# Kernel tuning notes

Hardware: AMD Instinct MI355X
Metric: run time of the kernel (lower is better)

Reference implementation:

```python
import jax, jax.numpy as jnp
import numpy as np

N, B, DIN = 128, 2, 128
D, DFF, NHEAD, NLAYERS = 256, 1024, 8, 2
BLOCK = 32
LENGTH = 160


def setup_inputs() -> dict:
    key = jax.random.key(0)
    ks = jax.random.split(key, 10)
    r = lambda k, sh: jax.random.normal(k, sh, jnp.float32) * 0.05
    return {
        "inputs": jax.random.normal(ks[0], (N, B, DIN), jnp.float32),
        "in_W1": r(ks[1], (DIN, DFF)), "in_b1": jnp.zeros((DFF,), jnp.float32),
        "in_W2": r(ks[2], (DFF, D)), "in_b2": jnp.zeros((D,), jnp.float32),
        "k_W1": r(ks[3], (DIN, DFF)), "k_b1": jnp.zeros((DFF,), jnp.float32),
        "k_W2": r(ks[4], (DFF, 2)), "k_b2": jnp.zeros((2,), jnp.float32),
        "Wqkv": r(ks[5], (NLAYERS, D, 3 * D)), "bqkv": jnp.zeros((NLAYERS, 3 * D), jnp.float32),
        "Wo": r(ks[6], (NLAYERS, D, D)), "bo": jnp.zeros((NLAYERS, D), jnp.float32),
        "ln1_g": jnp.ones((NLAYERS, D), jnp.float32), "ln1_b": jnp.zeros((NLAYERS, D), jnp.float32),
        "W1": r(ks[7], (NLAYERS, D, DFF)), "b1": jnp.zeros((NLAYERS, DFF), jnp.float32),
        "W2": r(ks[8], (NLAYERS, DFF, D)), "b2": jnp.zeros((NLAYERS, D), jnp.float32),
        "ln2_g": jnp.ones((NLAYERS, D), jnp.float32), "ln2_b": jnp.zeros((NLAYERS, D), jnp.float32),
        "length": LENGTH,
    }


def _ln(x, g, b):
    m = jnp.mean(x, axis=-1, keepdims=True)
    v = jnp.mean(jnp.square(x - m), axis=-1, keepdims=True)
    return (x - m) * jax.lax.rsqrt(v + 1e-5) * g + b


def _forward(inputs, in_W1, in_b1, in_W2, in_b2, k_W1, k_b1, k_W2, k_b2,
             Wqkv, bqkv, Wo, bo, ln1_g, ln1_b, W1, b1, W2, b2, ln2_g, ln2_b, length):
    n, b, din = inputs.shape
    d = in_W2.shape[1]
    H, dh = NHEAD, in_W2.shape[1] // NHEAD
    Wmax = 2 * BLOCK + 1
    L = length
    idx = jnp.arange(n)
    starts = jnp.maximum(0, idx - BLOCK)                 # [N]
    ends = jnp.minimum(L, idx + BLOCK + 1)               # [N]
    cols = starts[:, None] + jnp.arange(Wmax)[None, :]   # [N,Wmax] absolute column per window slot
    valid = cols < ends[:, None]                          # [N,Wmax] ragged-window mask

    # sinusoidal PE at absolute column positions (start_idx = max(0, i-block))
    pos = cols.astype(jnp.float32)
    div = jnp.exp(jnp.arange(0, din, 2, dtype=jnp.float32) * (-np.log(10000.0) / din))
    ang = pos[..., None] * div                            # [N,Wmax,din/2]
    pe = jnp.stack([jnp.sin(ang), jnp.cos(ang)], axis=-1).reshape(n, Wmax, din)

    # row token repeated across its window + PE, then input_ff
    x = inputs[:, None, :, :] + pe[:, :, None, :]         # [N,Wmax,B,din]
    h = jnp.maximum(x @ in_W1 + in_b1, 0.0) @ in_W2 + in_b2  # [N,Wmax,B,D]

    # TransformerEncoder (post-norm, relu, eval mode) over the window axis, padded slots masked as keys
    kmask = valid[:, None, None, None, :]                 # [N,1,1,1,Wmax]
    scale = 1.0 / np.sqrt(dh)
    for l in range(Wqkv.shape[0]):
        qkv = h @ Wqkv[l] + bqkv[l]
        q, k, v = [t.reshape(n, Wmax, b, H, dh) for t in jnp.split(qkv, 3, axis=-1)]
        s = jnp.einsum('nqbhe,nkbhe->nbhqk', q, k) * scale
        s = jnp.where(kmask, s, -jnp.inf)
        a = jax.nn.softmax(s, axis=-1)
        o = jnp.einsum('nbhqk,nkbhe->nqbhe', a, v).reshape(n, Wmax, b, d)
        h = _ln(h + o @ Wo[l] + bo[l], ln1_g[l], ln1_b[l])
        f = jnp.maximum(h @ W1[l] + b1[l], 0.0) @ W2[l] + b2[l]
        h = _ln(h + f, ln2_g[l], ln2_b[l])

    # hierarchy kernel scores (Gaussian band kernel with learned (mu, logsig) per row/batch)
    kp = jnp.maximum(inputs @ k_W1 + k_b1, 0.0) @ k_W2 + k_b2   # [N,B,2]
    hscale = L / n
    diff = cols.astype(jnp.float32) - idx[:, None].astype(jnp.float32) * hscale  # [N,Wmax]
    hier = -jnp.square(diff[:, :, None] - kp[:, None, :, 0]) * jnp.exp(kp[:, None, :, 1])  # [N,Wmax,B]

    # scatter banded values/scores into dense [N,L,...] then row-softmax and weighted combine
    n_idx = jnp.broadcast_to(idx[:, None], (n, Wmax))
    scat = jnp.where(valid, cols, L)                      # out-of-bounds -> dropped
    v_mat = jnp.zeros((n, L, b, d), jnp.float32).at[n_idx, scat].set(h, mode='drop')
    h_mat = jnp.full((n, L, b), -jnp.inf, jnp.float32).at[n_idx, scat].set(hier, mode='drop')
    w = jax.nn.softmax(h_mat, axis=0)[..., None]          # softmax over rows per column
    return jnp.sum(v_mat * w, axis=0)                     # [L,B,D]


def reference(inputs, in_W1, in_b1, in_W2, in_b2, k_W1, k_b1, k_W2, k_b2,
              Wqkv, bqkv, Wo, bo, ln1_g, ln1_b, W1, b1, W2, b2, ln2_g, ln2_b, length):
    return _forward(inputs, in_W1, in_b1, in_W2, in_b2, k_W1, k_b1, k_W2, k_b2,
                    Wqkv, bqkv, Wo, bo, ln1_g, ln1_b, W1, b1, W2, b2, ln2_g, ln2_b, length)
```

## Files before the change

### kernel.cpp

```cpp
#include <hip/hip_runtime.h>

constexpr int NN    = 128;
constexpr int BB    = 2;
constexpr int DIN   = 128;
constexpr int DD    = 256;
constexpr int DFF   = 1024;
constexpr int NH    = 8;
constexpr int DH    = 32;
constexpr int NL    = 2;
constexpr int BLK   = 32;
constexpr int WMAX  = 2 * BLK + 1;
constexpr int RROWS = NN * WMAX * BB;

typedef __attribute__((ext_vector_type(8))) short s16x8;
typedef __attribute__((ext_vector_type(4))) float f32x4;

__device__ __forceinline__ ushort f2bf(float f) {
  unsigned u = __float_as_uint(f);
  unsigned r = (u + 0x7fffu + ((u >> 16) & 1u)) >> 16;
  return (ushort)r;
}
__device__ __forceinline__ float bf2f(ushort h) {
  return __uint_as_float(((unsigned)h) << 16);
}
__device__ __forceinline__ float bfl(unsigned u) { return __uint_as_float(u << 16); }
__device__ __forceinline__ float bfh(unsigned u) { return __uint_as_float(u & 0xffff0000u); }

struct TD { const float* in; ushort* out; int K; int N; };
struct TPack { TD d[10]; };

__global__ __launch_bounds__(256) void k_wconv(TPack p) {
  TD t = p.d[blockIdx.y];
  int total = t.K * t.N;
  for (int i = blockIdx.x * 256 + threadIdx.x; i < total; i += gridDim.x * 256) {
    int n = i / t.K, k = i - n * t.K;
    t.out[i] = f2bf(t.in[(size_t)k * t.N + n]);
  }
}

__global__ __launch_bounds__(256) void k_buildx(const float* __restrict__ inp,
                                                ushort* __restrict__ x) {
  int e = blockIdx.x * 256 + threadIdx.x;
  int i = e & 127, r = e >> 7;
  int n = r / (WMAX * BB);
  int rem = r - n * (WMAX * BB);
  int w = rem >> 1, b = rem & 1;
  int st = n - BLK; if (st < 0) st = 0;
  float pos = (float)(st + w);
  float div = __expf(-0.0719557841f * (float)(i & 126));
  float ang = pos * div;
  float pe = (i & 1) ? __cosf(ang) : __sinf(ang);
  x[e] = f2bf(inp[(n * BB + b) * DIN + i] + pe);
}

__global__ __launch_bounds__(256) void k_kp(
    const float* __restrict__ inp, const float* __restrict__ kW1,
    const float* __restrict__ kb1, const float* __restrict__ kW2,
    const float* __restrict__ kb2, float* __restrict__ kp) {
  __shared__ float xs[DIN];
  __shared__ float red[8];
  int row = blockIdx.x;
  int tid = threadIdx.x;
  if (tid < DIN) xs[tid] = inp[row * DIN + tid];
  __syncthreads();
  float a0 = 0.f, a1 = 0.f;
  for (int j = tid; j < DFF; j += 256) {
    float acc = kb1[j];
    for (int k = 0; k < DIN; ++k) acc += xs[k] * kW1[k * DFF + j];
    acc = fmaxf(acc, 0.f);
    a0 += acc * kW2[2 * j];
    a1 += acc * kW2[2 * j + 1];
  }
#pragma unroll
  for (int m = 32; m > 0; m >>= 1) {
    a0 += __shfl_xor(a0, m, 64);
    a1 += __shfl_xor(a1, m, 64);
  }
  if ((tid & 63) == 0) { red[(tid >> 6) * 2] = a0; red[(tid >> 6) * 2 + 1] = a1; }
  __syncthreads();
  if (tid == 0) {
    kp[row * 2 + 0] = red[0] + red[2] + red[4] + red[6] + kb2[0];
    kp[row * 2 + 1] = red[1] + red[3] + red[5] + red[7] + kb2[1];
  }
}

constexpr int BM = 128, BN = 64, BK = 64;

template<int RELU, int HAS_RES>
__global__ __launch_bounds__(256) void k_gemm(
    const ushort* __restrict__ A, const ushort* __restrict__ Bt,
    const float* __restrict__ bias, const ushort* __restrict__ resid,
    ushort* __restrict__ out, int N, int K) {
  __shared__ __align__(16) char As[BM * BK * 2];
  __shared__ __align__(16) char Bs[BN * BK * 2];
  int tid = threadIdx.x;
  int m0 = blockIdx.x * BM, n0 = blockIdx.y * BN;
  int lane = tid & 63, w = tid >> 6;
  int wr = w >> 1, wc = w & 1;
  int fr = lane & 15, g = lane >> 4;
  f32x4 acc[4][2] = {};

  for (int kb = 0; kb < K; kb += BK) {
    __syncthreads();
#pragma unroll
    for (int it = 0; it < 4; ++it) {
      int e = tid + it * 256;
      int row = e >> 3, c = e & 7;
      uint4 v = *(const uint4*)(A + (size_t)(m0 + row) * K + kb + c * 8);
      int boff = (row * 128 + c * 16) ^ ((row & 7) << 4);
      *(uint4*)(As + boff) = v;
    }
#pragma unroll
    for (int it = 0; it < 2; ++it) {
      int e = tid + it * 256;
      int row = e >> 3, c = e & 7;
      uint4 v = *(const uint4*)(Bt + (size_t)(n0 + row) * K + kb + c * 8);
      int boff = (row * 128 + c * 16) ^ ((row & 7) << 4);
      *(uint4*)(Bs + boff) = v;
    }
    __syncthreads();
#pragma unroll
    for (int ks = 0; ks < 2; ++ks) {
      int kByte = ks * 64 + g * 16;
      s16x8 a[4], b[2];
#pragma unroll
      for (int m = 0; m < 4; ++m) {
        int row = wr * 64 + m * 16 + fr;
        a[m] = *(const s16x8*)(As + ((row * 128 + kByte) ^ ((row & 7) << 4)));
      }
#pragma unroll
      for (int n = 0; n < 2; ++n) {
        int row = wc * 32 + n * 16 + fr;
        b[n] = *(const s16x8*)(Bs + ((row * 128 + kByte) ^ ((row & 7) << 4)));
      }
#pragma unroll
      for (int m = 0; m < 4; ++m)
#pragma unroll
        for (int n = 0; n < 2; ++n)
          acc[m][n] = __builtin_amdgcn_mfma_f32_16x16x32_bf16(a[m], b[n], acc[m][n], 0, 0, 0);
    }
  }
#pragma unroll
  for (int m = 0; m < 4; ++m) {
    int row = m0 + wr * 64 + m * 16 + g * 4;
#pragma unroll
    for (int n = 0; n < 2; ++n) {
      int col = n0 + wc * 32 + n * 16 + fr;
      float bv = bias[col];
#pragma unroll
      for (int j = 0; j < 4; ++j) {
        float v = acc[m][n][j] + bv;
        if (HAS_RES) v += bf2f(resid[(size_t)(row + j) * N + col]);
        if (RELU) v = fmaxf(v, 0.f);
        out[(size_t)(row + j) * N + col] = f2bf(v);
      }
    }
  }
}

constexpr int QKS = 40;
constexpr int VTS = 104;
constexpr int PS  = 104;

__global__ __launch_bounds__(320) void k_attn(
    const ushort* __restrict__ qkv, ushort* __restrict__ o,
    const int* __restrict__ lenp) {
  __shared__ __align__(16) ushort Qs[80 * QKS];
  __shared__ __align__(16) ushort Ks[80 * QKS];
  __shared__ __align__(16) ushort Vt[32 * VTS];
  __shared__ __align__(16) ushort Pb[5 * 16 * PS];
  int L = lenp[0];
  int blk = blockIdx.x;
  int hh = blk & 7;
  int nb = blk >> 3;
  int b = nb & 1;
  int n = nb >> 1;
  int s0 = n - BLK; if (s0 < 0) s0 = 0;
  int e0 = n + BLK + 1; if (e0 > L) e0 = L;
  int vn = e0 - s0;
  int tid = threadIdx.x;

  for (int i = tid; i < 32 * VTS / 2; i += 320) ((uint*)Vt)[i] = 0;
  for (int i = tid; i < 15 * QKS / 2; i += 320) {
    ((uint*)(Qs + 65 * QKS))[i] = 0;
    ((uint*)(Ks + 65 * QKS))[i] = 0;
  }
  for (int e = tid; e < 65 * 4; e += 320) {
    int r = e >> 2, c = e & 3;
    const ushort* base = qkv + ((size_t)(n * WMAX + r) * BB + b) * (3 * DD) + hh * DH;
    *(uint4*)(Qs + r * QKS + c * 8) = *(const uint4*)(base + c * 8);
    *(uint4*)(Ks + r * QKS + c * 8) = *(const uint4*)(base + DD + c * 8);
    uint4 vv = *(const uint4*)(base + 2 * DD + c * 8);
    const ushort* vp = (const ushort*)&vv;
#pragma unroll
    for (int u = 0; u < 8; ++u) Vt[(c * 8 + u) * VTS + r] = vp[u];
  }
  __syncthreads();

  int w = tid >> 6, lane = tid & 63;
  int fr = lane & 15, g = lane >> 4;
  int q0 = w * 16;
  ushort* Pw = Pb + w * 16 * PS;

  s16x8 aq = *(const s16x8*)(Qs + (q0 + fr) * QKS + g * 8);
  f32x4 sacc[5];
#pragma unroll
  for (int t = 0; t < 5; ++t) {
    s16x8 bk = *(const s16x8*)(Ks + (t * 16 + fr) * QKS + g * 8);
    f32x4 z = {0.f, 0.f, 0.f, 0.f};
    sacc[t] = __builtin_amdgcn_mfma_f32_16x16x32_bf16(aq, bk, z, 0, 0, 0);
  }
  const float scl = 0.17677669529663687f;
#pragma unroll
  for (int j = 0; j < 4; ++j) {
    float pv[5];
    float mx = -3e38f;
#pragma unroll
    for (int t = 0; t < 5; ++t) {
      bool ok = (t * 16 + fr) < vn;
      pv[t] = ok ? sacc[t][j] * scl : -3e38f;
      mx = fmaxf(mx, pv[t]);
    }
#pragma unroll
    for (int d = 1; d < 16; d <<= 1) mx = fmaxf(mx, __shfl_xor(mx, d, 64));
    float sum = 0.f;
#pragma unroll
    for (int t = 0; t < 5; ++t) {
      float e = ((t * 16 + fr) < vn) ? __expf(pv[t] - mx) : 0.f;
      pv[t] = e;
      sum += e;
    }
#pragma unroll
    for (int d = 1; d < 16; d <<= 1) sum += __shfl_xor(sum, d, 64);
    float inv = 1.f / sum;
#pragma unroll
    for (int t = 0; t < 5; ++t)
      Pw[(g * 4 + j) * PS + t * 16 + fr] = f2bf(pv[t] * inv);
  }
  {
    int zr = lane >> 2, zc = 80 + (lane & 3) * 4;
    *(uint2*)(Pw + zr * PS + zc) = make_uint2(0u, 0u);
  }
  __syncthreads();

  f32x4 oacc[2] = {};
#pragma unroll
  for (int k0 = 0; k0 < 3; ++k0) {
    s16x8 ap = *(const s16x8*)(Pw + fr * PS + k0 * 32 + g * 8);
#pragma unroll
    for (int nt = 0; nt < 2; ++nt) {
      s16x8 bv = *(const s16x8*)(Vt + (nt * 16 + fr) * VTS + k0 * 32 + g * 8);
      oacc[nt] = __builtin_amdgcn_mfma_f32_16x16x32_bf16(ap, bv, oacc[nt], 0, 0, 0);
    }
  }
#pragma unroll
  for (int nt = 0; nt < 2; ++nt) {
#pragma unroll
    for (int j = 0; j < 4; ++j) {
      int qr = q0 + g * 4 + j;
      if (qr < WMAX)
        o[((size_t)(n * WMAX + qr) * BB + b) * DD + hh * DH + nt * 16 + fr] =
            f2bf(oacc[nt][j]);
    }
  }
}

__global__ __launch_bounds__(256) void k_ln(
    const ushort* __restrict__ z, const float* __restrict__ g,
    const float* __restrict__ be, ushort* __restrict__ h) {
  int row = blockIdx.x * 4 + (threadIdx.x >> 6);
  int lane = threadIdx.x & 63;
  const ushort* zr = z + (size_t)row * DD + lane * 4;
  uint2 pk = *(const uint2*)zr;
  float v0 = bfl(pk.x), v1 = bfh(pk.x), v2 = bfl(pk.y), v3 = bfh(pk.y);
  float sm = v0 + v1 + v2 + v3;
  float sq = v0 * v0 + v1 * v1 + v2 * v2 + v3 * v3;
#pragma unroll
  for (int m = 32; m > 0; m >>= 1) {
    sm += __shfl_xor(sm, m, 64);
    sq += __shfl_xor(sq, m, 64);
  }
  float mean = sm * (1.f / DD);
  float var = sq * (1.f / DD) - mean * mean;
  float rs = rsqrtf(var + 1e-5f);
  int c = lane * 4;
  float o0 = (v0 - mean) * rs * g[c] + be[c];
  float o1 = (v1 - mean) * rs * g[c + 1] + be[c + 1];
  float o2 = (v2 - mean) * rs * g[c + 2] + be[c + 2];
  float o3 = (v3 - mean) * rs * g[c + 3] + be[c + 3];
  uint2 outp;
  outp.x = (unsigned)f2bf(o0) | ((unsigned)f2bf(o1) << 16);
  outp.y = (unsigned)f2bf(o2) | ((unsigned)f2bf(o3) << 16);
  *(uint2*)(h + (size_t)row * DD + c) = outp;
}

__global__ __launch_bounds__(256) void k_final(
    const ushort* __restrict__ h, const float* __restrict__ kp,
    float* __restrict__ out, const int* __restrict__ lenp) {
  int L = lenp[0];
  int t = blockIdx.x >> 1, b = blockIdx.x & 1;
  float hsc = (float)L / (float)NN;
  int nlo = t - BLK; if (nlo < 0) nlo = 0;
  int nhi = t + BLK; if (nhi > NN - 1) nhi = NN - 1;
  float mx = -3e38f;
  for (int n = nlo; n <= nhi; ++n) {
    float kp0 = kp[(n * BB + b) * 2 + 0];
    float kp1 = kp[(n * BB + b) * 2 + 1];
    float dif = (float)t - (float)n * hsc - kp0;
    float lg = -dif * dif * __expf(kp1);
    mx = fmaxf(mx, lg);
  }
  float sum = 0.f, acc = 0.f;
  int c = threadIdx.x;
  for (int n = nlo; n <= nhi; ++n) {
    float kp0 = kp[(n * BB + b) * 2 + 0];
    float kp1 = kp[(n * BB + b) * 2 + 1];
    float dif = (float)t - (float)n * hsc - kp0;
    float lg = -dif * dif * __expf(kp1);
    float p = __expf(lg - mx);
    sum += p;
    int st = n - BLK; if (st < 0) st = 0;
    int w = t - st;
    acc += p * bf2f(h[(size_t)((n * WMAX + w) * BB + b) * DD + c]);
  }
  out[(size_t)(t * BB + b) * DD + c] = acc / sum;
}

extern "C" void kernel_launch(void* const* d_in, const int* in_sizes, int n_in,
                              void* d_out, int out_size, void* d_ws, size_t ws_size,
                              hipStream_t stream) {
  const float* inputs = (const float*)d_in[0];
  const float* in_W1  = (const float*)d_in[1];
  const float* in_b1  = (const float*)d_in[2];
  const float* in_W2  = (const float*)d_in[3];
  const float* in_b2  = (const float*)d_in[4];
  const float* k_W1   = (const float*)d_in[5];
  const float* k_b1   = (const float*)d_in[6];
  const float* k_W2   = (const float*)d_in[7];
  const float* k_b2   = (const float*)d_in[8];
  const float* Wqkv   = (const float*)d_in[9];
  const float* bqkv   = (const float*)d_in[10];
  const float* Wo     = (const float*)d_in[11];
  const float* bo     = (const float*)d_in[12];
  const float* ln1_g  = (const float*)d_in[13];
  const float* ln1_b  = (const float*)d_in[14];
  const float* W1     = (const float*)d_in[15];
  const float* b1     = (const float*)d_in[16];
  const float* W2     = (const float*)d_in[17];
  const float* b2     = (const float*)d_in[18];
  const float* ln2_g  = (const float*)d_in[19];
  const float* ln2_b  = (const float*)d_in[20];
  const int*   lenp   = (const int*)d_in[21];
  float* out = (float*)d_out;
  (void)in_sizes; (void)n_in; (void)ws_size;

  ushort* wsu = (ushort*)d_ws;
  size_t off = 0;
  auto alloc = [&](size_t nelem) { ushort* p = wsu + off; off += (nelem + 7) & ~7ull; return p; };
  ushort* inW1t = alloc((size_t)DFF * DIN);
  ushort* inW2t = alloc((size_t)DD * DFF);
  ushort* Wqkvt = alloc((size_t)NL * 3 * DD * DD);
  ushort* Wot   = alloc((size_t)NL * DD * DD);
  ushort* W1t   = alloc((size_t)NL * DFF * DD);
  ushort* W2t   = alloc((size_t)NL * DD * DFF);
  ushort* xz    = alloc((size_t)RROWS * DD);
  ushort* tq    = alloc((size_t)RROWS * DFF);
  ushort* hb    = alloc((size_t)RROWS * DD);
  ushort* ob    = alloc((size_t)RROWS * DD);
  float*  kp    = (float*)(wsu + off);

  int L = out_size / (BB * DD);

  TPack tp;
  tp.d[0] = {in_W1, inW1t, DIN, DFF};
  tp.d[1] = {in_W2, inW2t, DFF, DD};
  tp.d[2] = {Wqkv,                       Wqkvt,                     DD, 3 * DD};
  tp.d[3] = {Wqkv + (size_t)DD * 3 * DD, Wqkvt + (size_t)3 * DD * DD, DD, 3 * DD};
  tp.d[4] = {Wo,                    Wot,                  DD, DD};
  tp.d[5] = {Wo + (size_t)DD * DD,  Wot + (size_t)DD * DD, DD, DD};
  tp.d[6] = {W1,                     W1t,                   DD, DFF};
  tp.d[7] = {W1 + (size_t)DD * DFF,  W1t + (size_t)DFF * DD, DD, DFF};
  tp.d[8] = {W2,                     W2t,                   DFF, DD};
  tp.d[9] = {W2 + (size_t)DFF * DD,  W2t + (size_t)DD * DFF, DFF, DD};
  k_wconv<<<dim3(1024, 10), 256, 0, stream>>>(tp);

  k_buildx<<<RROWS * DIN / 256, 256, 0, stream>>>(inputs, xz);
  k_kp<<<NN * BB, 256, 0, stream>>>(inputs, k_W1, k_b1, k_W2, k_b2, kp);

  k_gemm<1, 0><<<dim3(RROWS / BM, DFF / BN), 256, 0, stream>>>(
      xz, inW1t, in_b1, nullptr, tq, DFF, DIN);
  k_gemm<0, 0><<<dim3(RROWS / BM, DD / BN), 256, 0, stream>>>(
      tq, inW2t, in_b2, nullptr, hb, DD, DFF);

  for (int l = 0; l < NL; ++l) {
    k_gemm<0, 0><<<dim3(RROWS / BM, 3 * DD / BN), 256, 0, stream>>>(
        hb, Wqkvt + (size_t)l * 3 * DD * DD, bqkv + (size_t)l * 3 * DD,
        nullptr, tq, 3 * DD, DD);
    k_attn<<<NN * BB * NH, 320, 0, stream>>>(tq, ob, lenp);
    k_gemm<0, 1><<<dim3(RROWS / BM, DD / BN), 256, 0, stream>>>(
        ob, Wot + (size_t)l * DD * DD, bo + (size_t)l * DD, hb, xz, DD, DD);
    k_ln<<<RROWS / 4, 256, 0, stream>>>(xz, ln1_g + (size_t)l * DD,
                                        ln1_b + (size_t)l * DD, hb);
    k_gemm<1, 0><<<dim3(RROWS / BM, DFF / BN), 256, 0, stream>>>(
        hb, W1t + (size_t)l * DFF * DD, b1 + (size_t)l * DFF, nullptr, tq, DFF, DD);
    k_gemm<0, 1><<<dim3(RROWS / BM, DD / BN), 256, 0, stream>>>(
        tq, W2t + (size_t)l * DD * DFF, b2 + (size_t)l * DD, hb, xz, DD, DFF);
    k_ln<<<RROWS / 4, 256, 0, stream>>>(xz, ln2_g + (size_t)l * DD,
                                        ln2_b + (size_t)l * DD, hb);
  }
  k_final<<<L * BB, 256, 0, stream>>>(hb, kp, out, lenp);
}
```

Baseline: 323.7 us.

## Fuse LayerNorm into full-width GEMM epilogue and retile GEMMs to 512 threads

Replaces the 256-thread 128x64 GEMM with a 512-thread kernel whose tiles span 256 output columns. For the output-projection and FFN-down GEMMs, each block then covers a whole 256-wide row, so the bias, residual add and LayerNorm run in the epilogue. This removes the separate k_ln launches and the intermediate xz round trip to global memory. The weight-conversion kernel also becomes a shared-memory tiled transpose for coalesced reads and writes. The cost is fewer blocks for the N=256 GEMMs, plus an in-place residual/output on hb that relies on each block reading its residual before the barrier and writing after it.

```diff
diff --git a/kernel.cpp b/kernel.cpp
--- a/kernel.cpp
+++ b/kernel.cpp
@@ -31,10 +31,23 @@
 
 __global__ __launch_bounds__(256) void k_wconv(TPack p) {
   TD t = p.d[blockIdx.y];
-  int total = t.K * t.N;
-  for (int i = blockIdx.x * 256 + threadIdx.x; i < total; i += gridDim.x * 256) {
-    int n = i / t.K, k = i - n * t.K;
-    t.out[i] = f2bf(t.in[(size_t)k * t.N + n]);
+  int ntk = t.K >> 5, ntn = t.N >> 5;
+  int tile = blockIdx.x;
+  if (tile >= ntk * ntn) return;
+  int tn = tile / ntk, tk = tile - tn * ntk;
+  __shared__ float ls[32 * 33];
+  int tid = threadIdx.x;
+  int r = tid >> 5, c = tid & 31;
+#pragma unroll
+  for (int i = 0; i < 4; ++i) {
+    int kk = r + 8 * i;
+    ls[kk * 33 + c] = t.in[(size_t)(tk * 32 + kk) * t.N + tn * 32 + c];
+  }
+  __syncthreads();
+#pragma unroll
+  for (int i = 0; i < 4; ++i) {
+    int rr = r + 8 * i;
+    t.out[(size_t)(tn * 32 + rr) * t.K + tk * 32 + c] = f2bf(ls[c * 33 + rr]);
   }
 }
 
@@ -84,75 +97,120 @@
   }
 }
 
-constexpr int BM = 128, BN = 64, BK = 64;
-
-template<int RELU, int HAS_RES>
-__global__ __launch_bounds__(256) void k_gemm(
+template<int BMT, int RELU, int FUSE_LN>
+__global__ __launch_bounds__(512) void k_gemm8(
     const ushort* __restrict__ A, const ushort* __restrict__ Bt,
     const float* __restrict__ bias, const ushort* __restrict__ resid,
+    const float* __restrict__ lng, const float* __restrict__ lnb,
     ushort* __restrict__ out, int N, int K) {
-  __shared__ __align__(16) char As[BM * BK * 2];
-  __shared__ __align__(16) char Bs[BN * BK * 2];
+  constexpr int MF = BMT / 32;
+  __shared__ __align__(16) char As[BMT * 128];
+  __shared__ __align__(16) char Bs[256 * 128];
+  __shared__ float psum[FUSE_LN ? 4 : 1][FUSE_LN ? BMT : 1];
+  __shared__ float psq [FUSE_LN ? 4 : 1][FUSE_LN ? BMT : 1];
   int tid = threadIdx.x;
-  int m0 = blockIdx.x * BM, n0 = blockIdx.y * BN;
+  int m0 = blockIdx.x * BMT, n0 = blockIdx.y * 256;
   int lane = tid & 63, w = tid >> 6;
-  int wr = w >> 1, wc = w & 1;
+  int wr = w >> 2, wc = w & 3;
   int fr = lane & 15, g = lane >> 4;
-  f32x4 acc[4][2] = {};
-
-  for (int kb = 0; kb < K; kb += BK) {
+  f32x4 acc[MF][4] = {};
+
+  for (int kb = 0; kb < K; kb += 64) {
     __syncthreads();
 #pragma unroll
-    for (int it = 0; it < 4; ++it) {
-      int e = tid + it * 256;
+    for (int it = 0; it < BMT / 64; ++it) {
+      int e = tid + it * 512;
       int row = e >> 3, c = e & 7;
       uint4 v = *(const uint4*)(A + (size_t)(m0 + row) * K + kb + c * 8);
-      int boff = (row * 128 + c * 16) ^ ((row & 7) << 4);
-      *(uint4*)(As + boff) = v;
-    }
-#pragma unroll
-    for (int it = 0; it < 2; ++it) {
-      int e = tid + it * 256;
+      *(uint4*)(As + ((row * 128 + c * 16) ^ ((row & 7) << 4))) = v;
+    }
+#pragma unroll
+    for (int it = 0; it < 4; ++it) {
+      int e = tid + it * 512;
       int row = e >> 3, c = e & 7;
       uint4 v = *(const uint4*)(Bt + (size_t)(n0 + row) * K + kb + c * 8);
-      int boff = (row * 128 + c * 16) ^ ((row & 7) << 4);
-      *(uint4*)(Bs + boff) = v;
+      *(uint4*)(Bs + ((row * 128 + c * 16) ^ ((row & 7) << 4))) = v;
     }
     __syncthreads();
 #pragma unroll
     for (int ks = 0; ks < 2; ++ks) {
       int kByte = ks * 64 + g * 16;
-      s16x8 a[4], b[2];
-#pragma unroll
-      for (int m = 0; m < 4; ++m) {
-        int row = wr * 64 + m * 16 + fr;
+      s16x8 a[MF], b[4];
+#pragma unroll
+      for (int m = 0; m < MF; ++m) {
+        int row = wr * (BMT / 2) + m * 16 + fr;
         a[m] = *(const s16x8*)(As + ((row * 128 + kByte) ^ ((row & 7) << 4)));
       }
 #pragma unroll
-      for (int n = 0; n < 2; ++n) {
-        int row = wc * 32 + n * 16 + fr;
+      for (int n = 0; n < 4; ++n) {
+        int row = wc * 64 + n * 16 + fr;
         b[n] = *(const s16x8*)(Bs + ((row * 128 + kByte) ^ ((row & 7) << 4)));
       }
 #pragma unroll
-      for (int m = 0; m < 4; ++m)
-#pragma unroll
-        for (int n = 0; n < 2; ++n)
+      for (int m = 0; m < MF; ++m)
+#pragma unroll
+        for (int n = 0; n < 4; ++n)
           acc[m][n] = __builtin_amdgcn_mfma_f32_16x16x32_bf16(a[m], b[n], acc[m][n], 0, 0, 0);
     }
   }
-#pragma unroll
-  for (int m = 0; m < 4; ++m) {
-    int row = m0 + wr * 64 + m * 16 + g * 4;
-#pragma unroll
-    for (int n = 0; n < 2; ++n) {
-      int col = n0 + wc * 32 + n * 16 + fr;
-      float bv = bias[col];
+
+  if constexpr (!FUSE_LN) {
+#pragma unroll
+    for (int m = 0; m < MF; ++m) {
+      int rowb = m0 + wr * (BMT / 2) + m * 16 + g * 4;
+#pragma unroll
+      for (int n = 0; n < 4; ++n) {
+        int col = n0 + wc * 64 + n * 16 + fr;
+        float bv = bias[col];
+#pragma unroll
+        for (int j = 0; j < 4; ++j) {
+          float v = acc[m][n][j] + bv;
+          if (RELU) v = fmaxf(v, 0.f);
+          out[(size_t)(rowb + j) * N + col] = f2bf(v);
+        }
+      }
+    }
+  } else {
+#pragma unroll
+    for (int m = 0; m < MF; ++m) {
+      int rowb = wr * (BMT / 2) + m * 16 + g * 4;
 #pragma unroll
       for (int j = 0; j < 4; ++j) {
-        float v = acc[m][n][j] + bv;
-        if (HAS_RES) v += bf2f(resid[(size_t)(row + j) * N + col]);
-        if (RELU) v = fmaxf(v, 0.f);
-        out[(size_t)(row + j) * N + col] = f2bf(v);
+        float ps = 0.f, pq = 0.f;
+#pragma unroll
+        for (int n = 0; n < 4; ++n) {
+          int col = wc * 64 + n * 16 + fr;
+          float v = acc[m][n][j] + bias[col]
+                  + bf2f(resid[(size_t)(m0 + rowb + j) * 256 + col]);
+          acc[m][n][j] = v;
+          ps += v; pq += v * v;
+        }
+#pragma unroll
+        for (int d = 1; d < 16; d <<= 1) {
+          ps += __shfl_xor(ps, d, 64);
+          pq += __shfl_xor(pq, d, 64);
+        }
+        if (fr == 0) { psum[wc][rowb + j] = ps; psq[wc][rowb + j] = pq; }
+      }
+    }
+    __syncthreads();
+#pragma unroll
+    for (int m = 0; m < MF; ++m) {
+      int rowb = wr * (BMT / 2) + m * 16 + g * 4;
+#pragma unroll
+      for (int j = 0; j < 4; ++j) {
+        int lr = rowb + j;
+        float sm = psum[0][lr] + psum[1][lr] + psum[2][lr] + psum[3][lr];
+        float sq = psq[0][lr] + psq[1][lr] + psq[2][lr] + psq[3][lr];
+        float mean = sm * (1.f / 256.f);
+        float var = sq * (1.f / 256.f) - mean * mean;
+        float rs = rsqrtf(var + 1e-5f);
+#pragma unroll
+        for (int n = 0; n < 4; ++n) {
+          int col = wc * 64 + n * 16 + fr;
+          float v = (acc[m][n][j] - mean) * rs * lng[col] + lnb[col];
+          out[(size_t)(m0 + lr) * 256 + col] = f2bf(v);
+        }
       }
     }
   }
@@ -263,35 +321,6 @@
             f2bf(oacc[nt][j]);
     }
   }
-}
-
-__global__ __launch_bounds__(256) void k_ln(
-    const ushort* __restrict__ z, const float* __restrict__ g,
-    const float* __restrict__ be, ushort* __restrict__ h) {
-  int row = blockIdx.x * 4 + (threadIdx.x >> 6);
-  int lane = threadIdx.x & 63;
-  const ushort* zr = z + (size_t)row * DD + lane * 4;
-  uint2 pk = *(const uint2*)zr;
-  float v0 = bfl(pk.x), v1 = bfh(pk.x), v2 = bfl(pk.y), v3 = bfh(pk.y);
-  float sm = v0 + v1 + v2 + v3;
-  float sq = v0 * v0 + v1 * v1 + v2 * v2 + v3 * v3;
-#pragma unroll
-  for (int m = 32; m > 0; m >>= 1) {
-    sm += __shfl_xor(sm, m, 64);
-    sq += __shfl_xor(sq, m, 64);
-  }
-  float mean = sm * (1.f / DD);
-  float var = sq * (1.f / DD) - mean * mean;
-  float rs = rsqrtf(var + 1e-5f);
-  int c = lane * 4;
-  float o0 = (v0 - mean) * rs * g[c] + be[c];
-  float o1 = (v1 - mean) * rs * g[c + 1] + be[c + 1];
-  float o2 = (v2 - mean) * rs * g[c + 2] + be[c + 2];
-  float o3 = (v3 - mean) * rs * g[c + 3] + be[c + 3];
-  uint2 outp;
-  outp.x = (unsigned)f2bf(o0) | ((unsigned)f2bf(o1) << 16);
-  outp.y = (unsigned)f2bf(o2) | ((unsigned)f2bf(o3) << 16);
-  *(uint2*)(h + (size_t)row * DD + c) = outp;
 }
 
 __global__ __launch_bounds__(256) void k_final(
@@ -363,7 +392,7 @@
   ushort* Wot   = alloc((size_t)NL * DD * DD);
   ushort* W1t   = alloc((size_t)NL * DFF * DD);
   ushort* W2t   = alloc((size_t)NL * DD * DFF);
-  ushort* xz    = alloc((size_t)RROWS * DD);
+  ushort* x     = alloc((size_t)RROWS * DIN);
   ushort* tq    = alloc((size_t)RROWS * DFF);
   ushort* hb    = alloc((size_t)RROWS * DD);
   ushort* ob    = alloc((size_t)RROWS * DD);
@@ -374,39 +403,38 @@
   TPack tp;
   tp.d[0] = {in_W1, inW1t, DIN, DFF};
   tp.d[1] = {in_W2, inW2t, DFF, DD};
-  tp.d[2] = {Wqkv,                       Wqkvt,                     DD, 3 * DD};
-  tp.d[3] = {Wqkv + (size_t)DD * 3 * DD, Wqkvt + (size_t)3 * DD * DD, DD, 3 * DD};
-  tp.d[4] = {Wo,                    Wot,                  DD, DD};
+  tp.d[2] = {Wqkv,                        Wqkvt,                       DD, 3 * DD};
+  tp.d[3] = {Wqkv + (size_t)DD * 3 * DD,  Wqkvt + (size_t)3 * DD * DD, DD, 3 * DD};
+  tp.d[4] = {Wo,                    Wot,                   DD, DD};
   tp.d[5] = {Wo + (size_t)DD * DD,  Wot + (size_t)DD * DD, DD, DD};
-  tp.d[6] = {W1,                     W1t,                   DD, DFF};
-  tp.d[7] = {W1 + (size_t)DD * DFF,  W1t + (size_t)DFF * DD, DD, DFF};
-  tp.d[8] = {W2,                     W2t,                   DFF, DD};
-  tp.d[9] = {W2 + (size_t)DFF * DD,  W2t + (size_t)DD * DFF, DFF, DD};
-  k_wconv<<<dim3(1024, 10), 256, 0, stream>>>(tp);
-
-  k_buildx<<<RROWS * DIN / 256, 256, 0, stream>>>(inputs, xz);
+  tp.d[6] = {W1,                      W1t,                    DD, DFF};
+  tp.d[7] = {W1 + (size_t)DD * DFF,   W1t + (size_t)DFF * DD, DD, DFF};
+  tp.d[8] = {W2,                      W2t,                    DFF, DD};
+  tp.d[9] = {W2 + (size_t)DFF * DD,   W2t + (size_t)DD * DFF, DFF, DD};
+  k_wconv<<<dim3(256, 10), 256, 0, stream>>>(tp);
+
+  k_buildx<<<RROWS * DIN / 256, 256, 0, stream>>>(inputs, x);
   k_kp<<<NN * BB, 256, 0, stream>>>(inputs, k_W1, k_b1, k_W2, k_b2, kp);
 
-  k_gemm<1, 0><<<dim3(RROWS / BM, DFF / BN), 256, 0, stream>>>(
-      xz, inW1t, in_b1, nullptr, tq, DFF, DIN);
-  k_gemm<0, 0><<<dim3(RROWS / BM, DD / BN), 256, 0, stream>>>(
-      tq, inW2t, in_b2, nullptr, hb, DD, DFF);
+  k_gemm8<128, 1, 0><<<dim3(RROWS / 128, 4), 512, 0, stream>>>(
+      x, inW1t, in_b1, nullptr, nullptr, nullptr, tq, DFF, DIN);
+  k_gemm8<64, 0, 0><<<dim3(RROWS / 64, 1), 512, 0, stream>>>(
+      tq, inW2t, in_b2, nullptr, nullptr, nullptr, hb, DD, DFF);
 
   for (int l = 0; l < NL; ++l) {
-    k_gemm<0, 0><<<dim3(RROWS / BM, 3 * DD / BN), 256, 0, stream>>>(
+    k_gemm8<128, 0, 0><<<dim3(RROWS / 128, 3), 512, 0, stream>>>(
         hb, Wqkvt + (size_t)l * 3 * DD * DD, bqkv + (size_t)l * 3 * DD,
-        nullptr, tq, 3 * DD, DD);
+        nullptr, nullptr, nullptr, tq, 3 * DD, DD);
     k_attn<<<NN * BB * NH, 320, 0, stream>>>(tq, ob, lenp);
-    k_gemm<0, 1><<<dim3(RROWS / BM, DD / BN), 256, 0, stream>>>(
-        ob, Wot + (size_t)l * DD * DD, bo + (size_t)l * DD, hb, xz, DD, DD);
-    k_ln<<<RROWS / 4, 256, 0, stream>>>(xz, ln1_g + (size_t)l * DD,
-                                        ln1_b + (size_t)l * DD, hb);
-    k_gemm<1, 0><<<dim3(RROWS / BM, DFF / BN), 256, 0, stream>>>(
-        hb, W1t + (size_t)l * DFF * DD, b1 + (size_t)l * DFF, nullptr, tq, DFF, DD);
-    k_gemm<0, 1><<<dim3(RROWS / BM, DD / BN), 256, 0, stream>>>(
-        tq, W2t + (size_t)l * DD * DFF, b2 + (size_t)l * DD, hb, xz, DD, DFF);
-    k_ln<<<RROWS / 4, 256, 0, stream>>>(xz, ln2_g + (size_t)l * DD,
-                                        ln2_b + (size_t)l * DD, hb);
+    k_gemm8<64, 0, 1><<<dim3(RROWS / 64, 1), 512, 0, stream>>>(
+        ob, Wot + (size_t)l * DD * DD, bo + (size_t)l * DD, hb,
+        ln1_g + (size_t)l * DD, ln1_b + (size_t)l * DD, hb, DD, DD);
+    k_gemm8<128, 1, 0><<<dim3(RROWS / 128, 4), 512, 0, stream>>>(
+        hb, W1t + (size_t)l * DFF * DD, b1 + (size_t)l * DFF,
+        nullptr, nullptr, nullptr, tq, DFF, DD);
+    k_gemm8<64, 0, 1><<<dim3(RROWS / 64, 1), 512, 0, stream>>>(
+        tq, W2t + (size_t)l * DD * DFF, b2 + (size_t)l * DD, hb,
+        ln2_g + (size_t)l * DD, ln2_b + (size_t)l * DD, hb, DD, DFF);
   }
   k_final<<<L * BB, 256, 0, stream>>>(hb, kp, out, lenp);
 }
```

New measurement: 296.6 us. 1.09x faster.
